# Kernel tuning notes

Hardware: AMD Instinct MI355X
Metric: run time of the kernel (lower is better)

The kernel has to match this reference:

```python
import jax, jax.numpy as jnp
import numpy as np

B, DIM, H, W = 2, 384, 256, 256
HID = DIM * 1          # ffn_expansion_factor = 1 (required for source code to be consistent)
P = 8                  # patch_size


def setup_inputs() -> dict:
    key = jax.random.key(0)
    k0, k1, k2, k3, k4 = jax.random.split(key, 5)
    x = jax.random.normal(k0, (B, DIM, H, W), jnp.float32)
    # learned spectral filter: (hidden, P, P//2+1), real-valued, multiplies rfft2 coeffs
    fft_filter = jax.random.normal(k1, (HID, P, P // 2 + 1), jnp.float32)
    # project_in: 1x1 conv dim->hidden, weight (out,in)
    w_in = jax.random.normal(k2, (HID, DIM), jnp.float32) * (1.0 / np.sqrt(DIM))
    # depthwise 3x3 conv, groups=channels, weight (C,1,3,3)
    w_dw = jax.random.normal(k3, (HID, 1, 3, 3), jnp.float32) * (1.0 / 3.0)
    # project_out: 1x1 conv hidden//2 -> dim
    w_out = jax.random.normal(k4, (DIM, HID // 2), jnp.float32) * (1.0 / np.sqrt(HID // 2))
    return {"x": x, "fft_filter": fft_filter, "w_in": w_in, "w_dw": w_dw, "w_out": w_out}


def reference(x, fft_filter, w_in, w_dw, w_out):
    b, c, h, w = x.shape
    hid = w_in.shape[0]
    hb, wb = h // P, w // P
    # project_in (1x1 conv == channel GEMM)
    t = jnp.einsum('bchw,oc->bohw', x, w_in)
    # patchify into 8x8 blocks and apply per-patch 2D real FFT spectral filter.
    # reshape b c (hb p1) (wb p2) -> b c hb p1 wb p2; FFT over axes (3,5).
    tp = t.reshape(b, hid, hb, P, wb, P)
    tf = jnp.fft.rfft2(tp, axes=(3, 5))                 # (b,hid,hb,P,wb,P//2+1) complex
    tf = tf * fft_filter[None, :, None, :, None, :]
    tp = jnp.fft.irfft2(tf, s=(P, P), axes=(3, 5))
    t = tp.reshape(b, hid, h, w)
    # depthwise 3x3 conv, stride 1, padding 1
    t = jax.lax.conv_general_dilated(
        t, w_dw, window_strides=(1, 1), padding='SAME',
        feature_group_count=hid,
        dimension_numbers=('NCHW', 'OIHW', 'NCHW'))
    # gated GELU (exact erf gelu, matching torch F.gelu default)
    x1, x2 = t[:, : hid // 2], t[:, hid // 2:]
    g = jax.nn.gelu(x1, approximate=False) * x2
    # project_out (1x1 conv)
    return jnp.einsum('bchw,oc->bohw', g, w_out)
```

## Files before the change

### kernel.cpp

```cpp
#include <hip/hip_runtime.h>
#include <hip/hip_bf16.h>
#include <math.h>

#define BB 2
#define DIM 384
#define HID 384
#define HW 65536

typedef short s16x8 __attribute__((ext_vector_type(8)));
typedef short s16x4 __attribute__((ext_vector_type(4)));
typedef __bf16 bf16x8 __attribute__((ext_vector_type(8)));
typedef float f32x4 __attribute__((ext_vector_type(4)));

__device__ inline short f2b(float f) {
    __hip_bfloat16 h = __float2bfloat16(f);
    return __builtin_bit_cast(short, h);
}
__device__ inline float b2f(short s) {
    return __bfloat162float(__builtin_bit_cast(__hip_bfloat16, s));
}

__device__ inline void gl_lds16(const short* g, short* l) {
    __builtin_amdgcn_global_load_lds(
        (const __attribute__((address_space(1))) unsigned int*)g,
        (__attribute__((address_space(3))) unsigned int*)l, 16, 0, 0);
}

__global__ void k_prep(const float* __restrict__ w_in, const float* __restrict__ w_out,
                       const float* __restrict__ F,
                       short* __restrict__ wbin, short* __restrict__ wbout,
                       float* __restrict__ Dtc, short* __restrict__ Rb) {
    int i = blockIdx.x * 256 + threadIdx.x;
    if (i < 147456) { wbin[i] = f2b(w_in[i]); return; }
    i -= 147456;
    if (i < 73728) { wbout[i] = f2b(w_out[i]); return; }
    i -= 73728;
    if (i < 24576) {
        int c = i >> 6, j = i & 63;
        int a = j >> 3, q = j & 7;
        float d;
        if (q >= 1 && q <= 3)
            d = F[c * 40 + a * 5 + q];
        else if (q >= 5)
            d = F[c * 40 + ((8 - a) & 7) * 5 + (8 - q)];
        else
            d = 0.5f * (F[c * 40 + a * 5 + q] + F[c * 40 + ((8 - a) & 7) * 5 + q]);
        Dtc[i] = d * (1.f / 64.f);
        return;
    }
    i -= 24576;
    if (i < 4096) {
        int j = i >> 6, k = i & 63;
        const float cas[8] = {1.f, 1.41421356237f, 1.f, 0.f, -1.f, -1.41421356237f, -1.f, 0.f};
        int t = ((j >> 3) * (k >> 3) + (j & 7) * (k & 7)) & 7;
        Rb[i] = f2b(cas[t]);
    }
}

__global__ __launch_bounds__(256) void k_cvtx(const float* __restrict__ X, short* __restrict__ Xt) {
    int hw0 = blockIdx.x * 64, c0 = blockIdx.y * 64, b = blockIdx.z;
    __shared__ __align__(16) short S[64 * 64];
    int t = threadIdx.x;
    const float* Xb = X + ((size_t)(b * DIM) << 16);
    short* Xtb = Xt + (size_t)b * HW * DIM;
#pragma unroll
    for (int p = 0; p < 2; ++p) {
        int row = p * 32 + (t >> 3), sb = t & 7;
        const float* src = &Xb[((size_t)(c0 + row) << 16) + hw0 + sb * 8];
        float4 a = *(const float4*)src;
        float4 bq = *(const float4*)(src + 4);
        s16x8 v;
        v[0] = f2b(a.x);  v[1] = f2b(a.y);  v[2] = f2b(a.z);  v[3] = f2b(a.w);
        v[4] = f2b(bq.x); v[5] = f2b(bq.y); v[6] = f2b(bq.z); v[7] = f2b(bq.w);
        *(s16x8*)&S[row * 64 + ((sb ^ (row >> 3)) << 3)] = v;
    }
    __syncthreads();
    int h = hw0 >> 8, wb0 = hw0 & 255;
#pragma unroll
    for (int p = 0; p < 2; ++p) {
        int row = p * 32 + (t >> 3), ch = t & 7;
        s16x8 v;
#pragma unroll
        for (int j = 0; j < 8; ++j)
            v[j] = S[(ch * 8 + j) * 64 + (row ^ (ch << 3))];
        int wv = wb0 + row;
        int rowp = (((h >> 3) << 5) + (wv >> 3)) * 64 + ((h & 7) << 3) + (wv & 7);
        *(s16x8*)&Xtb[(size_t)rowp * DIM + c0 + ch * 8] = v;
    }
}

__global__ __launch_bounds__(256) void k_gemm1c(const short* __restrict__ W,
                                                const short* __restrict__ Xt,
                                                const short* __restrict__ Rb,
                                                const float* __restrict__ Dtc,
                                                short* __restrict__ T) {
    __shared__ __align__(16) short SH[17408 + 4096];
    short* Rs = SH + 17408;
    int d = blockIdx.x;
    int wg = (d & 7) * 192 + (d >> 3);
    int m0 = (wg % 3) * 128;
    int tx = wg / 3;
    int pid0 = tx * 2;
    int b  = blockIdx.z;
    int tid = threadIdx.x;
    int lane = tid & 63, w = tid >> 6;
    int wr = w >> 1, wc = w & 1;
    int lm = lane & 15, quad = lane >> 4;

    {
        int j0 = tid >> 3, kb0 = tid & 7;
        gl_lds16(Rb + j0 * 64 + ((kb0 ^ (j0 & 7)) << 3), Rs + tid * 8);
        int t2 = tid + 256;
        int j1 = t2 >> 3, kb1 = t2 & 7;
        gl_lds16(Rb + j1 * 64 + ((kb1 ^ (j1 & 7)) << 3), Rs + t2 * 8);
    }

    const short* Xbase = Xt + ((size_t)b * HW + (size_t)pid0 * 64) * DIM;

    f32x4 acc[4][4];
#pragma unroll
    for (int i = 0; i < 4; ++i)
#pragma unroll
        for (int j = 0; j < 4; ++j) acc[i][j] = 0.f;

    int grow = tid >> 2, gseg = tid & 3;
    int gsw = (grow >> 1) & 3;
    int gcol = ((gseg ^ gsw) << 3);
#pragma unroll
    for (int q = 0; q < 2; ++q) {
        int G = q * 256 + tid;
        int row = grow + q * 64;
        int col = ((gseg ^ ((row >> 1) & 3)) << 3);
        gl_lds16(Xbase + (size_t)row * DIM + col, SH + G * 8);
        gl_lds16(W + (size_t)(m0 + row) * DIM + col, SH + 4096 + G * 8);
    }
    __syncthreads();

    int fsw = (lm >> 1) & 3;
    for (int kc = 0; kc < 12; ++kc) {
        if (kc < 11) {
            int k0 = (kc + 1) * 32;
            int nb = ((kc + 1) & 1) * 8192;
#pragma unroll
            for (int q = 0; q < 2; ++q) {
                int G = q * 256 + tid;
                int row = grow + q * 64;
                int col = k0 + ((gseg ^ ((row >> 1) & 3)) << 3);
                gl_lds16(Xbase + (size_t)row * DIM + col, SH + nb + G * 8);
                gl_lds16(W + (size_t)(m0 + row) * DIM + col, SH + nb + 4096 + G * 8);
            }
        }
        const short* Xs = SH + (kc & 1) * 8192;
        const short* Ws = Xs + 4096;
        int csw = ((quad ^ fsw) << 3);
        bf16x8 af[4], bfr[4];
#pragma unroll
        for (int i = 0; i < 4; ++i)
            af[i] = __builtin_bit_cast(bf16x8, *(const s16x8*)&Xs[(wr * 64 + i * 16 + lm) * 32 + csw]);
#pragma unroll
        for (int j = 0; j < 4; ++j)
            bfr[j] = __builtin_bit_cast(bf16x8, *(const s16x8*)&Ws[(wc * 64 + j * 16 + lm) * 32 + csw]);
#pragma unroll
        for (int i = 0; i < 4; ++i)
#pragma unroll
            for (int j = 0; j < 4; ++j)
                acc[i][j] = __builtin_amdgcn_mfma_f32_16x16x32_bf16(af[i], bfr[j], acc[i][j], 0, 0, 0);
        __syncthreads();
    }

#pragma unroll
    for (int i = 0; i < 4; ++i)
#pragma unroll
        for (int j = 0; j < 4; ++j) {
            s16x4 v4;
#pragma unroll
            for (int r = 0; r < 4; ++r) v4[r] = f2b(acc[i][j][r]);
            *(s16x4*)&SH[(wc * 64 + j * 16 + lm) * 136 + wr * 64 + i * 16 + quad * 4] = v4;
        }

    f32x4 acc2[4][4];
#pragma unroll
    for (int i = 0; i < 4; ++i)
#pragma unroll
        for (int j = 0; j < 4; ++j) acc2[i][j] = 0.f;
#pragma unroll
    for (int ks = 0; ks < 2; ++ks) {
        int csw = (((ks * 4 + quad) ^ (lm & 7)) << 3);
        bf16x8 af[4], bfr[4];
#pragma unroll
        for (int i = 0; i < 4; ++i)
            af[i] = __builtin_bit_cast(bf16x8, *(const s16x8*)&Rs[(i * 16 + lm) * 64 + csw]);
#pragma unroll
        for (int j = 0; j < 4; ++j)
            bfr[j] = __builtin_bit_cast(bf16x8,
                *(const s16x8*)&SH[(wc * 64 + j * 16 + lm) * 136 + wr * 64 + ks * 32 + quad * 8]);
#pragma unroll
        for (int i = 0; i < 4; ++i)
#pragma unroll
            for (int j = 0; j < 4; ++j)
                acc2[i][j] = __builtin_amdgcn_mfma_f32_16x16x32_bf16(af[i], bfr[j], acc2[i][j], 0, 0, 0);
    }
#pragma unroll
    for (int i = 0; i < 4; ++i)
#pragma unroll
        for (int j2 = 0; j2 < 4; ++j2) {
            float4 dv = *(const float4*)&Dtc[(size_t)(m0 + wc * 64 + j2 * 16 + lm) * 64 + i * 16 + quad * 4];
            s16x4 v4;
            v4[0] = f2b(acc2[i][j2][0] * dv.x);
            v4[1] = f2b(acc2[i][j2][1] * dv.y);
            v4[2] = f2b(acc2[i][j2][2] * dv.z);
            v4[3] = f2b(acc2[i][j2][3] * dv.w);
            *(s16x4*)&SH[(wc * 64 + j2 * 16 + lm) * 136 + wr * 64 + i * 16 + quad * 4] = v4;
        }

    f32x4 acc3[4][4];
#pragma unroll
    for (int i = 0; i < 4; ++i)
#pragma unroll
        for (int j = 0; j < 4; ++j) acc3[i][j] = 0.f;
#pragma unroll
    for (int ks = 0; ks < 2; ++ks) {
        int csw = (((ks * 4 + quad) ^ (lm & 7)) << 3);
        bf16x8 af[4], bfr[4];
#pragma unroll
        for (int i = 0; i < 4; ++i)
            af[i] = __builtin_bit_cast(bf16x8, *(const s16x8*)&Rs[(i * 16 + lm) * 64 + csw]);
#pragma unroll
        for (int j = 0; j < 4; ++j)
            bfr[j] = __builtin_bit_cast(bf16x8,
                *(const s16x8*)&SH[(wc * 64 + j * 16 + lm) * 136 + wr * 64 + ks * 32 + quad * 8]);
#pragma unroll
        for (int i = 0; i < 4; ++i)
#pragma unroll
            for (int j = 0; j < 4; ++j)
                acc3[i][j] = __builtin_amdgcn_mfma_f32_16x16x32_bf16(af[i], bfr[j], acc3[i][j], 0, 0, 0);
    }
#pragma unroll
    for (int i = 0; i < 4; ++i)
#pragma unroll
        for (int j2 = 0; j2 < 4; ++j2) {
            s16x4 v4;
#pragma unroll
            for (int r = 0; r < 4; ++r) v4[r] = f2b(acc3[i][j2][r]);
            *(s16x4*)&SH[(wc * 64 + j2 * 16 + lm) * 136 + wr * 64 + i * 16 + quad * 4] = v4;
        }
    __syncthreads();
#pragma unroll
    for (int kq = 0; kq < 8; ++kq) {
        int idx = kq * 256 + tid;
        int row = idx >> 4, seg = idx & 15;
        s16x8 vv = *(const s16x8*)&SH[row * 136 + seg * 8];
        *(s16x8*)&T[(((size_t)(b * HID + m0 + row)) << 16) + pid0 * 64 + seg * 8] = vv;
    }
}

__global__ __launch_bounds__(256) void k_dwgt(const short* __restrict__ Y,
                                              const float* __restrict__ Wdw,
                                              short* __restrict__ Gt) {
    int bz = blockIdx.z;
    int b  = bz / 24;
    int cg = bz % 24;
    int c0 = cg * 8;
    int h0 = blockIdx.y * 16, w0 = blockIdx.x * 64;
    __shared__ __align__(16) short S[16][18][80];
    __shared__ float sw[16][9];
    int tid = threadIdx.x;
    if (tid < 144) {
        int p = tid / 9, j = tid % 9;
        int ch = (p < 8) ? (c0 + p) : (c0 + p - 8 + 192);
        sw[p][j] = Wdw[ch * 9 + j];
    }
    for (int t = tid; t < 2880; t += 256) {
        int v = t % 10, r = (t / 10) % 18, p = t / 180;
        int gh = h0 + r - 1;
        int gw = w0 + v * 8 - 8;
        int ch = (p < 8) ? (c0 + p) : (c0 + p - 8 + 192);
        s16x8 val = {0, 0, 0, 0, 0, 0, 0, 0};
        if (gh >= 0 && gh < 256 && gw >= 0 && gw <= 248) {
            int pid = ((gh >> 3) << 5) + (gw >> 3);
            val = *(const s16x8*)&Y[((size_t)(b * HID + ch) << 16) + (pid << 6) + ((gh & 7) << 3)];
        }
        *(s16x8*)&S[p][r][v * 8] = val;
    }
    __syncthreads();
    s16x8 ov[4];
#pragma unroll
    for (int it = 0; it < 4; ++it) {
        int idx = it * 256 + tid;
        int p = idx >> 7, run = idx & 127;
        int r = run >> 3, c8 = (run & 7) * 8;
        float z1[8], z2[8];
#pragma unroll
        for (int k = 0; k < 8; ++k) { z1[k] = 0.f; z2[k] = 0.f; }
#pragma unroll
        for (int i = 0; i < 3; ++i) {
            {
                s16x4 wv[4];
#pragma unroll
                for (int q = 0; q < 4; ++q) wv[q] = *(const s16x4*)&S[p][r + i][c8 + 4 + q * 4];
                float fv[10];
#pragma unroll
                for (int q = 0; q < 10; ++q) fv[q] = b2f(wv[(q + 3) >> 2][(q + 3) & 3]);
#pragma unroll
                for (int j = 0; j < 3; ++j) {
                    float wgt = sw[p][i * 3 + j];
#pragma unroll
                    for (int k = 0; k < 8; ++k) z1[k] += fv[k + j] * wgt;
                }
            }
            {
                s16x4 wv[4];
#pragma unroll
                for (int q = 0; q < 4; ++q) wv[q] = *(const s16x4*)&S[p + 8][r + i][c8 + 4 + q * 4];
                float fv[10];
#pragma unroll
                for (int q = 0; q < 10; ++q) fv[q] = b2f(wv[(q + 3) >> 2][(q + 3) & 3]);
#pragma unroll
                for (int j = 0; j < 3; ++j) {
                    float wgt = sw[p + 8][i * 3 + j];
#pragma unroll
                    for (int k = 0; k < 8; ++k) z2[k] += fv[k + j] * wgt;
                }
            }
        }
#pragma unroll
        for (int k = 0; k < 8; ++k) {
            float g = 0.5f * z1[k] * (1.f + erff(z1[k] * 0.70710678118654752f));
            ov[it][k] = f2b(g * z2[k]);
        }
    }
    __syncthreads();
    short* Ob = (short*)S;
#pragma unroll
    for (int it = 0; it < 4; ++it) {
        int idx = it * 256 + tid;
        int p = idx >> 7, run = idx & 127;
        int pos = (run >> 3) * 64 + (run & 7) * 8;
#pragma unroll
        for (int k = 0; k < 8; ++k)
            Ob[(pos + k) * 9 + p] = ov[it][k];
    }
    __syncthreads();
    short* Gb = Gt + (((size_t)(b * 24 + cg)) << 16) * 8;
#pragma unroll
    for (int it = 0; it < 4; ++it) {
        int pos = it * 256 + tid;
        int r = pos >> 6, cl = pos & 63;
        s16x8 v;
#pragma unroll
        for (int k = 0; k < 8; ++k) v[k] = Ob[pos * 9 + k];
        *(s16x8*)&Gb[(size_t)(((h0 + r) << 8) + w0 + cl) * 8] = v;
    }
}

__global__ __launch_bounds__(256) void k_gemm_bf16(const short* __restrict__ A,
                                                   const short* __restrict__ Bt,
                                                   float* __restrict__ C,
                                                   int N, int K) {
    __shared__ __align__(16) short SH[16384];
    const short* Bz = Bt + (size_t)blockIdx.z * (size_t)N * K;
    float* Cz = C + (size_t)blockIdx.z * (size_t)384 * N;
    int d = blockIdx.x;
    int wg = (d & 7) * 192 + (d >> 3);
    int m0 = (wg % 3) * 128;
    int n0 = (wg / 3) * 128;
    int tid = threadIdx.x;
    int lane = tid & 63, w = tid >> 6;
    int wr = w >> 1, wc = w & 1;
    int lm = lane & 15, quad = lane >> 4;

    f32x4 acc[4][4];
#pragma unroll
    for (int i = 0; i < 4; ++i)
#pragma unroll
        for (int j = 0; j < 4; ++j) acc[i][j] = 0.f;

    int grow = tid >> 2, gseg = tid & 3;
#pragma unroll
    for (int q = 0; q < 2; ++q) {
        int row = grow + q * 64;
        int G = q * 256 + tid;
        int sg = gseg ^ ((row >> 1) & 3);
        gl_lds16(A + (size_t)(m0 + row) * K + (sg << 3), SH + G * 8);
        gl_lds16(Bz + ((size_t)sg * HW + n0 + row) * 8, SH + 4096 + G * 8);
    }
    __syncthreads();

    int fsw = (lm >> 1) & 3;
    for (int kc = 0; kc < 6; ++kc) {
        if (kc < 5) {
            int k0 = (kc + 1) * 32;
            int nb = ((kc + 1) & 1) * 8192;
#pragma unroll
            for (int q = 0; q < 2; ++q) {
                int row = grow + q * 64;
                int G = q * 256 + tid;
                int sg = gseg ^ ((row >> 1) & 3);
                gl_lds16(A + (size_t)(m0 + row) * K + k0 + (sg << 3), SH + nb + G * 8);
                gl_lds16(Bz + ((size_t)((k0 >> 3) + sg) * HW + n0 + row) * 8, SH + nb + 4096 + G * 8);
            }
        }
        const short* As = SH + (kc & 1) * 8192;
        const short* Bs = As + 4096;
        int csw = ((quad ^ fsw) << 3);
        bf16x8 af[4], bfr[4];
#pragma unroll
        for (int i = 0; i < 4; ++i)
            af[i] = __builtin_bit_cast(bf16x8, *(const s16x8*)&As[(wr * 64 + i * 16 + lm) * 32 + csw]);
#pragma unroll
        for (int j = 0; j < 4; ++j)
            bfr[j] = __builtin_bit_cast(bf16x8, *(const s16x8*)&Bs[(wc * 64 + j * 16 + lm) * 32 + csw]);
#pragma unroll
        for (int i = 0; i < 4; ++i)
#pragma unroll
            for (int j = 0; j < 4; ++j)
                acc[i][j] = __builtin_amdgcn_mfma_f32_16x16x32_bf16(af[i], bfr[j], acc[i][j], 0, 0, 0);
        __syncthreads();
    }
#pragma unroll
    for (int i = 0; i < 4; ++i) {
        int r0 = m0 + wr * 64 + i * 16 + quad * 4;
#pragma unroll
        for (int j = 0; j < 4; ++j) {
            int cidx = n0 + wc * 64 + j * 16 + lm;
#pragma unroll
            for (int r = 0; r < 4; ++r)
                Cz[(size_t)(r0 + r) * N + cidx] = acc[i][j][r];
        }
    }
}

extern "C" void kernel_launch(void* const* d_in, const int* in_sizes, int n_in,
                              void* d_out, int out_size, void* d_ws, size_t ws_size,
                              hipStream_t stream) {
    const float* x     = (const float*)d_in[0];
    const float* ff    = (const float*)d_in[1];
    const float* w_in  = (const float*)d_in[2];
    const float* w_dw  = (const float*)d_in[3];
    const float* w_out = (const float*)d_in[4];
    float* out = (float*)d_out;

    char* ws = (char*)d_ws;
    float* Dtc  = (float*)ws;
    short* wbin = (short*)(ws + 98304);
    short* wbout = (short*)(ws + 393216);
    short* Rbuf = (short*)(ws + 540672);
    short* bufA = (short*)(ws + 548864);
    short* bufB = (short*)(ws + 548864 + (size_t)100663296);
    short* Gt = bufA;

    k_prep<<<976, 256, 0, stream>>>(w_in, w_out, ff, wbin, wbout, Dtc, Rbuf);

    k_cvtx<<<dim3(HW / 64, DIM / 64, BB), 256, 0, stream>>>(x, bufA);

    k_gemm1c<<<dim3(1536, 1, BB), 256, 0, stream>>>(wbin, bufA, Rbuf, Dtc, bufB);

    k_dwgt<<<dim3(4, 16, BB * 24), 256, 0, stream>>>(bufB, w_dw, Gt);

    k_gemm_bf16<<<dim3(1536, 1, BB), 256, 0, stream>>>(wbout, Gt, out, HW, 192);
}
```

Before: 568.3 us.

## Triple-buffer activation tiles and use one barrier per k-step in GEMMs

```diff
diff --git a/kernel.cpp b/kernel.cpp
--- a/kernel.cpp
+++ b/kernel.cpp
@@ -94,8 +94,8 @@
                                                 const short* __restrict__ Rb,
                                                 const float* __restrict__ Dtc,
                                                 short* __restrict__ T) {
-    __shared__ __align__(16) short SH[17408 + 4096];
-    short* Rs = SH + 17408;
+    __shared__ __align__(16) short SH[24576];
+    short* Rs = SH + 20480;
     int d = blockIdx.x;
     int wg = (d & 7) * 192 + (d >> 3);
     int m0 = (wg % 3) * 128;
@@ -124,34 +124,47 @@
         for (int j = 0; j < 4; ++j) acc[i][j] = 0.f;
 
     int grow = tid >> 2, gseg = tid & 3;
-    int gsw = (grow >> 1) & 3;
-    int gcol = ((gseg ^ gsw) << 3);
 #pragma unroll
     for (int q = 0; q < 2; ++q) {
         int G = q * 256 + tid;
         int row = grow + q * 64;
         int col = ((gseg ^ ((row >> 1) & 3)) << 3);
         gl_lds16(Xbase + (size_t)row * DIM + col, SH + G * 8);
-        gl_lds16(W + (size_t)(m0 + row) * DIM + col, SH + 4096 + G * 8);
-    }
-    __syncthreads();
+        gl_lds16(W + (size_t)(m0 + row) * DIM + col, SH + 12288 + G * 8);
+    }
 
     int fsw = (lm >> 1) & 3;
+#pragma unroll
     for (int kc = 0; kc < 12; ++kc) {
         if (kc < 11) {
             int k0 = (kc + 1) * 32;
-            int nb = ((kc + 1) & 1) * 8192;
+            short* xb = SH + ((kc + 1) % 3) * 4096;
 #pragma unroll
             for (int q = 0; q < 2; ++q) {
                 int G = q * 256 + tid;
                 int row = grow + q * 64;
                 int col = k0 + ((gseg ^ ((row >> 1) & 3)) << 3);
-                gl_lds16(Xbase + (size_t)row * DIM + col, SH + nb + G * 8);
-                gl_lds16(W + (size_t)(m0 + row) * DIM + col, SH + nb + 4096 + G * 8);
-            }
-        }
-        const short* Xs = SH + (kc & 1) * 8192;
-        const short* Ws = Xs + 4096;
+                gl_lds16(Xbase + (size_t)row * DIM + col, xb + G * 8);
+            }
+            asm volatile("s_waitcnt vmcnt(2)" ::: "memory");
+        } else {
+            asm volatile("s_waitcnt vmcnt(0)" ::: "memory");
+        }
+        __builtin_amdgcn_s_barrier();
+        asm volatile("" ::: "memory");
+        if (kc < 11) {
+            int k0 = (kc + 1) * 32;
+            short* wb = SH + 12288 + ((kc + 1) & 1) * 4096;
+#pragma unroll
+            for (int q = 0; q < 2; ++q) {
+                int G = q * 256 + tid;
+                int row = grow + q * 64;
+                int col = k0 + ((gseg ^ ((row >> 1) & 3)) << 3);
+                gl_lds16(W + (size_t)(m0 + row) * DIM + col, wb + G * 8);
+            }
+        }
+        const short* Xs = SH + (kc % 3) * 4096;
+        const short* Ws = SH + 12288 + (kc & 1) * 4096;
         int csw = ((quad ^ fsw) << 3);
         bf16x8 af[4], bfr[4];
 #pragma unroll
@@ -160,13 +173,15 @@
 #pragma unroll
         for (int j = 0; j < 4; ++j)
             bfr[j] = __builtin_bit_cast(bf16x8, *(const s16x8*)&Ws[(wc * 64 + j * 16 + lm) * 32 + csw]);
+        __builtin_amdgcn_s_setprio(1);
 #pragma unroll
         for (int i = 0; i < 4; ++i)
 #pragma unroll
             for (int j = 0; j < 4; ++j)
                 acc[i][j] = __builtin_amdgcn_mfma_f32_16x16x32_bf16(af[i], bfr[j], acc[i][j], 0, 0, 0);
-        __syncthreads();
-    }
+        __builtin_amdgcn_s_setprio(0);
+    }
+    __syncthreads();
 
 #pragma unroll
     for (int i = 0; i < 4; ++i)
@@ -357,7 +372,7 @@
                                                    const short* __restrict__ Bt,
                                                    float* __restrict__ C,
                                                    int N, int K) {
-    __shared__ __align__(16) short SH[16384];
+    __shared__ __align__(16) short SH[20480];
     const short* Bz = Bt + (size_t)blockIdx.z * (size_t)N * K;
     float* Cz = C + (size_t)blockIdx.z * (size_t)384 * N;
     int d = blockIdx.x;
@@ -381,27 +396,42 @@
         int row = grow + q * 64;
         int G = q * 256 + tid;
         int sg = gseg ^ ((row >> 1) & 3);
-        gl_lds16(A + (size_t)(m0 + row) * K + (sg << 3), SH + G * 8);
-        gl_lds16(Bz + ((size_t)sg * HW + n0 + row) * 8, SH + 4096 + G * 8);
-    }
-    __syncthreads();
+        gl_lds16(Bz + ((size_t)sg * HW + n0 + row) * 8, SH + G * 8);
+        gl_lds16(A + (size_t)(m0 + row) * K + (sg << 3), SH + 12288 + G * 8);
+    }
 
     int fsw = (lm >> 1) & 3;
+#pragma unroll
     for (int kc = 0; kc < 6; ++kc) {
         if (kc < 5) {
             int k0 = (kc + 1) * 32;
-            int nb = ((kc + 1) & 1) * 8192;
+            short* bb = SH + ((kc + 1) % 3) * 4096;
 #pragma unroll
             for (int q = 0; q < 2; ++q) {
                 int row = grow + q * 64;
                 int G = q * 256 + tid;
                 int sg = gseg ^ ((row >> 1) & 3);
-                gl_lds16(A + (size_t)(m0 + row) * K + k0 + (sg << 3), SH + nb + G * 8);
-                gl_lds16(Bz + ((size_t)((k0 >> 3) + sg) * HW + n0 + row) * 8, SH + nb + 4096 + G * 8);
-            }
-        }
-        const short* As = SH + (kc & 1) * 8192;
-        const short* Bs = As + 4096;
+                gl_lds16(Bz + ((size_t)((k0 >> 3) + sg) * HW + n0 + row) * 8, bb + G * 8);
+            }
+            asm volatile("s_waitcnt vmcnt(2)" ::: "memory");
+        } else {
+            asm volatile("s_waitcnt vmcnt(0)" ::: "memory");
+        }
+        __builtin_amdgcn_s_barrier();
+        asm volatile("" ::: "memory");
+        if (kc < 5) {
+            int k0 = (kc + 1) * 32;
+            short* ab = SH + 12288 + ((kc + 1) & 1) * 4096;
+#pragma unroll
+            for (int q = 0; q < 2; ++q) {
+                int row = grow + q * 64;
+                int G = q * 256 + tid;
+                int sg = gseg ^ ((row >> 1) & 3);
+                gl_lds16(A + (size_t)(m0 + row) * K + k0 + (sg << 3), ab + G * 8);
+            }
+        }
+        const short* Bs = SH + (kc % 3) * 4096;
+        const short* As = SH + 12288 + (kc & 1) * 4096;
         int csw = ((quad ^ fsw) << 3);
         bf16x8 af[4], bfr[4];
 #pragma unroll
@@ -410,12 +440,13 @@
 #pragma unroll
         for (int j = 0; j < 4; ++j)
             bfr[j] = __builtin_bit_cast(bf16x8, *(const s16x8*)&Bs[(wc * 64 + j * 16 + lm) * 32 + csw]);
+        __builtin_amdgcn_s_setprio(1);
 #pragma unroll
         for (int i = 0; i < 4; ++i)
 #pragma unroll
             for (int j = 0; j < 4; ++j)
                 acc[i][j] = __builtin_amdgcn_mfma_f32_16x16x32_bf16(af[i], bfr[j], acc[i][j], 0, 0, 0);
-        __syncthreads();
+        __builtin_amdgcn_s_setprio(0);
     }
 #pragma unroll
     for (int i = 0; i < 4; ++i) {
```

Measured after the change: 563.4 us. Within noise of the previous version (-0.9%).
